# Kernel tuning notes

Hardware: AMD Instinct MI355X
Metric: run time of the kernel (lower is better)

The kernel has to match this reference:

```python
import jax, jax.numpy as jnp
import numpy as np

H, W = 16, 16  # input_resolution
NUM_HEADS = 16
DIM = 512


def build_relative_position_index(h, w):
    coords = np.stack(np.meshgrid(np.arange(h), np.arange(w), indexing='ij'))  # [2,h,w]
    cf = coords.reshape(2, -1)
    rel = cf[:, :, None] - cf[:, None, :]            # [2,N,N]
    rel = rel.transpose(1, 2, 0).astype(np.int32)    # [N,N,2]
    rel[:, :, 0] += h - 1
    rel[:, :, 1] += w - 1
    rel[:, :, 0] *= 2 * w - 1
    return jnp.asarray(rel.sum(-1).reshape(-1), dtype=jnp.int32)  # [N*N]


def setup_inputs() -> dict:
    key = jax.random.key(0)
    ks = jax.random.split(key, 6)
    B, N, C = 128, H * W, DIM
    x = jax.random.normal(ks[0], (B, N, C), dtype=jnp.float32)
    qkv_w = jax.random.normal(ks[1], (3 * C, C), dtype=jnp.float32) * (C ** -0.5)
    qkv_b = jax.random.normal(ks[2], (3 * C,), dtype=jnp.float32) * 0.02
    proj_w = jax.random.normal(ks[3], (C, C), dtype=jnp.float32) * (C ** -0.5)
    proj_b = jax.random.normal(ks[4], (C,), dtype=jnp.float32) * 0.02
    bias_table = jax.random.normal(ks[5], ((2 * H - 1) * (2 * W - 1), NUM_HEADS), dtype=jnp.float32) * 0.02
    rel_index = build_relative_position_index(H, W)
    return {"x": x, "qkv_w": qkv_w, "qkv_b": qkv_b, "proj_w": proj_w,
            "proj_b": proj_b, "bias_table": bias_table, "rel_index": rel_index}


def reference(x, qkv_w, qkv_b, proj_w, proj_b, bias_table, rel_index):
    B, N, C = x.shape
    h = NUM_HEADS
    hd = C // h
    scale = hd ** -0.5
    # qkv projection: [B,N,3C] -> [3,B,h,N,hd]
    qkv = (jnp.einsum('bnc,oc->bno', x, qkv_w) + qkv_b)
    qkv = qkv.reshape(B, N, 3, h, hd).transpose(2, 0, 3, 1, 4)
    q, k, v = qkv[0], qkv[1], qkv[2]
    # relative position bias: gather [N*N,h] -> [1,h,N,N]
    bias = bias_table[rel_index].reshape(N, N, h).transpose(2, 0, 1)[None]
    attn = jnp.einsum('bhnd,bhmd->bhnm', q * scale, k) + bias
    attn = jax.nn.softmax(attn, axis=-1)
    out = jnp.einsum('bhnm,bhmd->bhnd', attn, v)     # [B,h,N,hd]
    out = out.transpose(0, 2, 1, 3).reshape(B, N, C)
    return jnp.einsum('bnc,oc->bno', out, proj_w) + proj_b
```

## Files before the change

### kernel.cpp

```cpp
#include <hip/hip_runtime.h>

typedef __bf16 bf16_t;
typedef __bf16 bf16x4 __attribute__((ext_vector_type(4)));
typedef __bf16 bf16x8 __attribute__((ext_vector_type(8)));
typedef float f32x4 __attribute__((ext_vector_type(4)));

#define MFMA_16x16x32(a, b, c) __builtin_amdgcn_mfma_f32_16x16x32_bf16((a), (b), (c), 0, 0, 0)
#define LOG2E 1.4426950408889634f

__device__ inline bf16x8 cvt8(const float* __restrict__ p) {
  bf16x8 r;
#pragma unroll
  for (int j = 0; j < 8; j++) r[j] = (bf16_t)p[j];
  return r;
}

__device__ inline void load_lds16(const bf16_t* g, bf16_t* l) {
  __builtin_amdgcn_global_load_lds(
      (const __attribute__((address_space(1))) void*)g,
      (__attribute__((address_space(3))) void*)l, 16, 0, 0);
}

__global__ __launch_bounds__(256) void prep_k(
    const float* __restrict__ x, const float* __restrict__ qkv_w,
    const float* __restrict__ proj_w, const float* __restrict__ table,
    const int* __restrict__ rel,
    bf16_t* __restrict__ xbf, bf16_t* __restrict__ wqkvbf,
    bf16_t* __restrict__ wprojbf, float* __restrict__ biasws) {
  const int bid = blockIdx.x;
  if (bid < 8704) {
    size_t base = ((size_t)bid * 256 + threadIdx.x) * 8;
    if (base < 16777216) {
      *(bf16x8*)(xbf + base) = cvt8(x + base);
    } else if (base < 17563648) {
      size_t o = base - 16777216;
      *(bf16x8*)(wqkvbf + o) = cvt8(qkv_w + o);
    } else {
      size_t o = base - 17563648;
      *(bf16x8*)(wprojbf + o) = cvt8(proj_w + o);
    }
  } else {
    int idx = (bid - 8704) * 256 + threadIdx.x;
    int h = idx >> 16;
    int rem = idx & 65535;
    int rb = rem >> 12;
    int ct = (rem >> 8) & 15;
    int L = (rem >> 2) & 63;
    int r = idx & 3;
    int row = rb * 16 + (L >> 4) * 4 + r;
    int col = ct * 16 + (L & 15);
    biasws[idx] = table[rel[row * 256 + col] * 16 + h] * LOG2E;
  }
}

#define PH_OPEN() __builtin_amdgcn_s_setprio(1)

#define PH_CLOSE()                                        \
  do {                                                    \
    __builtin_amdgcn_s_setprio(0);                        \
    asm volatile("s_waitcnt lgkmcnt(0)" ::: "memory");    \
    __builtin_amdgcn_sched_barrier(0);                    \
    __builtin_amdgcn_s_barrier();                         \
    __builtin_amdgcn_sched_barrier(0);                    \
  } while (0)

#define GATE4()                                           \
  do {                                                    \
    __builtin_amdgcn_s_setprio(0);                        \
    asm volatile("s_waitcnt vmcnt(4)" ::: "memory");      \
    __builtin_amdgcn_s_barrier();                         \
    __builtin_amdgcn_sched_barrier(0);                    \
  } while (0)

#define GATE0()                                           \
  do {                                                    \
    __builtin_amdgcn_s_setprio(0);                        \
    asm volatile("s_waitcnt vmcnt(0)" ::: "memory");      \
    __builtin_amdgcn_s_barrier();                         \
    __builtin_amdgcn_sched_barrier(0);                    \
  } while (0)

#define STG2(src, dst, c)                                                        \
  do {                                                                           \
    load_lds16((src) + (c)*16384, (dst) + (c)*2048);                             \
    load_lds16((src) + ((c) + 1) * 16384, (dst) + ((c) + 1) * 2048);             \
  } while (0)

#define RDA2(dst, buf, ibase)                                                    \
  _Pragma("unroll") for (int i = 0; i < 2; ++i) {                                \
    dst[i][0] = *(const bf16x8*)&As[(buf)*8192 + a0 + ((ibase) + i) * 1024];     \
    dst[i][1] = *(const bf16x8*)&As[(buf)*8192 + a1 + ((ibase) + i) * 1024];     \
  }
#define RDB2(dst, buf, jbase)                                                    \
  _Pragma("unroll") for (int j = 0; j < 2; ++j) {                                \
    dst[j][0] = *(const bf16x8*)&Bs[(buf)*8192 + b0 + ((jbase) + j) * 1024];     \
    dst[j][1] = *(const bf16x8*)&Bs[(buf)*8192 + b1 + ((jbase) + j) * 1024];     \
  }

#define MFQ2(Af, Bf, I0, J0)                                                     \
  _Pragma("unroll") for (int i = 0; i < 2; ++i) _Pragma("unroll")                \
      for (int j = 0; j < 2; ++j) {                                              \
    acc[(I0) + i][(J0) + j] =                                                    \
        MFMA_16x16x32(Af[i][0], Bf[j][0], acc[(I0) + i][(J0) + j]);              \
    acc[(I0) + i][(J0) + j] =                                                    \
        MFMA_16x16x32(Af[i][1], Bf[j][1], acc[(I0) + i][(J0) + j]);              \
  }

#define GEMM_SETUP(Ap, Wp)                                                       \
  __shared__ bf16_t As[2 * 8192];                                                \
  __shared__ bf16_t Bs[2 * 8192];                                                \
  const int t = threadIdx.x;                                                     \
  const int w = t >> 6, L = t & 63;                                              \
  const int wm = w >> 1, wn = w & 1;                                             \
  const int lrow = L & 15, lq = L >> 4;                                          \
  const int srow = t >> 3;                                                       \
  const int sslot = (t & 7) ^ (srow & 7);                                        \
  const bf16_t* ga = (Ap) + (size_t)(m0 + srow) * 512 + sslot * 8;               \
  const bf16_t* gb = (Wp) + (size_t)(n0 + srow) * 512 + sslot * 8;               \
  bf16_t* la = As + t * 8;                                                       \
  bf16_t* lb = Bs + t * 8;                                                       \
  const int m8 = (lrow & 7) * 8;                                                 \
  const int a0 = (wm * 64 + lrow) * 64 + ((lq * 8) ^ m8);                        \
  const int a1 = (wm * 64 + lrow) * 64 + ((32 + lq * 8) ^ m8);                   \
  const int b0 = (wn * 64 + lrow) * 64 + ((lq * 8) ^ m8);                        \
  const int b1 = (wn * 64 + lrow) * 64 + ((32 + lq * 8) ^ m8);

#define PROLOGUE()                                                               \
  STG2(ga, la, 0); STG2(ga, la, 2);                                              \
  STG2(gb, lb, 0); STG2(gb, lb, 2);                                              \
  STG2(ga + 64, la + 8192, 0); STG2(ga + 64, la + 8192, 2);                      \
  asm volatile("s_waitcnt vmcnt(4)" ::: "memory");                               \
  __builtin_amdgcn_s_barrier();                                                  \
  __builtin_amdgcn_sched_barrier(0);

#define HALF_STEADY(CUR, LBDST, LADST, GBP, GAP)                                 \
  {                                                                              \
    bf16x8 fal[2][2], fbl[2][2], fah[2][2], fbh[2][2];                           \
    RDA2(fal, CUR, 0); RDB2(fbl, CUR, 0); RDB2(fbh, CUR, 2);                     \
    STG2(GBP, LBDST, 0);                                                         \
    PH_OPEN(); MFQ2(fal, fbl, 0, 0); PH_CLOSE();                                 \
    RDA2(fah, CUR, 2);                                                           \
    STG2(GBP, LBDST, 2);                                                         \
    PH_OPEN(); MFQ2(fal, fbh, 0, 2); PH_CLOSE();                                 \
    STG2(GAP, LADST, 0);                                                         \
    PH_OPEN(); MFQ2(fah, fbh, 2, 2); PH_CLOSE();                                 \
    STG2(GAP, LADST, 2);                                                         \
    PH_OPEN(); MFQ2(fah, fbl, 2, 0); GATE4();                                    \
  }

#define GEMM_LOOP()                                                              \
  {                                                                              \
    const bf16_t* gA = ga + 128;                                       \
    const bf16_t* gB = gb + 64;                                        \
    _Pragma("unroll 1") for (int G = 0; G < 3; ++G) {                            \
      HALF_STEADY(0, lb + 8192, la, gB, gA)                                      \
      HALF_STEADY(1, lb, la + 8192, gB + 64, gA + 64)                            \
      gA += 128; gB += 128;                                                      \
    }                                                                            \
    {            \
      bf16x8 fal[2][2], fbl[2][2], fah[2][2], fbh[2][2];                         \
      RDA2(fal, 0, 0); RDB2(fbl, 0, 0); RDB2(fbh, 0, 2);                         \
      STG2(gB, lb + 8192, 0);                                                    \
      PH_OPEN(); MFQ2(fal, fbl, 0, 0); PH_CLOSE();                               \
      RDA2(fah, 0, 2);                                                           \
      STG2(gB, lb + 8192, 2);                                                    \
      PH_OPEN(); MFQ2(fal, fbh, 0, 2); PH_CLOSE();                               \
      PH_OPEN(); MFQ2(fah, fbh, 2, 2); PH_CLOSE();                               \
      PH_OPEN(); MFQ2(fah, fbl, 2, 0); GATE0();                                  \
    }                                                                            \
    {                               \
      bf16x8 fal[2][2], fbl[2][2], fah[2][2], fbh[2][2];                         \
      RDA2(fal, 1, 0); RDB2(fbl, 1, 0); RDB2(fbh, 1, 2);                         \
      PH_OPEN(); MFQ2(fal, fbl, 0, 0); PH_CLOSE();                               \
      RDA2(fah, 1, 2);                                                           \
      PH_OPEN(); MFQ2(fal, fbh, 0, 2); PH_CLOSE();                               \
      PH_OPEN(); MFQ2(fah, fbh, 2, 2); PH_CLOSE();                               \
      PH_OPEN(); MFQ2(fah, fbl, 2, 0);                                           \
      __builtin_amdgcn_s_setprio(0);                                             \
      __builtin_amdgcn_sched_barrier(0);                                         \
    }                                                                            \
  }

__global__ __launch_bounds__(256, 2) void qkv_gemm128_k(
    const bf16_t* __restrict__ A, const bf16_t* __restrict__ W,
    const float* __restrict__ Bvec,
    bf16_t* __restrict__ qws, bf16_t* __restrict__ kws, bf16_t* __restrict__ vws) {
  const int id = blockIdx.x;
  const int wg = (id & 7) * 384 + (id >> 3);
  const int mt = wg / 12, nt = wg % 12;
  const int m0 = mt * 128, n0 = nt * 128;

  GEMM_SETUP(A, W);

  f32x4 acc[4][4];
#pragma unroll
  for (int jj = 0; jj < 4; ++jj) {
    float bv = Bvec[n0 + wn * 64 + jj * 16 + lrow];
#pragma unroll
    for (int i = 0; i < 4; ++i) acc[i][jj] = (f32x4){bv, bv, bv, bv};
  }

  PROLOGUE();
  GEMM_LOOP();

  const int col0 = n0 + wn * 64;
  const int s = col0 >> 9;
  bf16_t* dst = (s == 0) ? qws : (s == 1) ? kws : vws;
  const float mul = (s == 0) ? 0.17677669529663687f * LOG2E : 1.0f;
#pragma unroll
  for (int jj = 0; jj < 4; ++jj) {
    int o = col0 + jj * 16 + lrow;
    int rem = o & 511;
    int hh = rem >> 5, d = rem & 31;
#pragma unroll
    for (int i = 0; i < 4; ++i) {
#pragma unroll
      for (int r = 0; r < 4; ++r) {
        int m = m0 + wm * 64 + i * 16 + lq * 4 + r;
        int b = m >> 8, n = m & 255;
        dst[(size_t)(((b * 16 + hh) * 256 + n) << 5) + d] =
            (bf16_t)(acc[i][jj][r] * mul);
      }
    }
  }
}

__global__ __launch_bounds__(256, 2) void proj_gemm128_k(
    const bf16_t* __restrict__ A, const bf16_t* __restrict__ W,
    const float* __restrict__ Bvec, float* __restrict__ out) {
  const int id = blockIdx.x;
  const int wg = (id & 7) * 128 + (id >> 3);
  const int mt = wg >> 2, nt = wg & 3;
  const int m0 = mt * 128, n0 = nt * 128;

  GEMM_SETUP(A, W);

  f32x4 acc[4][4];
#pragma unroll
  for (int jj = 0; jj < 4; ++jj) {
    float bv = Bvec[n0 + wn * 64 + jj * 16 + lrow];
#pragma unroll
    for (int i = 0; i < 4; ++i) acc[i][jj] = (f32x4){bv, bv, bv, bv};
  }

  PROLOGUE();
  GEMM_LOOP();

#pragma unroll
  for (int jj = 0; jj < 4; ++jj) {
    int o = n0 + wn * 64 + jj * 16 + lrow;
#pragma unroll
    for (int i = 0; i < 4; ++i) {
#pragma unroll
      for (int r = 0; r < 4; ++r) {
        int m = m0 + wm * 64 + i * 16 + lq * 4 + r;
        out[(size_t)m * 512 + o] = acc[i][jj][r];
      }
    }
  }
}

__global__ __launch_bounds__(256) void attn_k(
    const bf16_t* __restrict__ qws, const bf16_t* __restrict__ kws,
    const bf16_t* __restrict__ vws, const float* __restrict__ biasws,
    bf16_t* __restrict__ aows) {
  __shared__ __align__(16) char smem[33792 + 16896];
  bf16_t* Ps = (bf16_t*)smem;
  bf16_t* Vs = (bf16_t*)(smem + 33792);

  const int id = blockIdx.x;
  const int xcd = id & 7;
  const int jj = id >> 3;
  const int bh = (jj >> 2) * 8 + xcd;
  const int strip = jj & 3;
  const int h = bh & 15, b = bh >> 4;

  const int t = threadIdx.x;
  const int w = t >> 6, L = t & 63;
  const int lrow = L & 15, lq = L >> 4;

  const bf16_t* kbase = kws + (size_t)bh * 8192;
  const bf16_t* vbase = vws + (size_t)bh * 8192;
#pragma unroll
  for (int c = 0; c < 4; c++) {
    bf16x8 vv = *(const bf16x8*)(vbase + t * 32 + c * 8);
#pragma unroll
    for (int j = 0; j < 8; j++) Vs[(c * 8 + j) * 264 + t] = vv[j];
  }

  const bf16_t* qbase = qws + (size_t)bh * 8192 + (strip * 64 + w * 16) * 32;
  bf16x8 qf = *(const bf16x8*)(qbase + lrow * 32 + lq * 8);
  bf16x8 kf[16];
#pragma unroll
  for (int ct = 0; ct < 16; ct++)
    kf[ct] = *(const bf16x8*)(kbase + (ct * 16 + lrow) * 32 + lq * 8);

  const float* bb = biasws + h * 65536 + (strip * 4 + w) * 4096;
  f32x4 S[16];
  __builtin_amdgcn_s_setprio(1);
#pragma unroll
  for (int ct = 0; ct < 16; ct++) {
    f32x4 bi = *(const f32x4*)(bb + ct * 256 + L * 4);
    S[ct] = MFMA_16x16x32(qf, kf[ct], bi);
  }
  __builtin_amdgcn_s_setprio(0);

  float sm[4] = {0.f, 0.f, 0.f, 0.f};
#pragma unroll
  for (int ct = 0; ct < 16; ct++)
#pragma unroll
    for (int r = 0; r < 4; r++) {
      float e;
      asm("v_exp_f32 %0, %1" : "=v"(e) : "v"(S[ct][r]));
      S[ct][r] = e;
      sm[r] += e;
    }
#pragma unroll
  for (int r = 0; r < 4; r++)
#pragma unroll
    for (int msk = 1; msk < 16; msk <<= 1)
      sm[r] += __shfl_xor(sm[r], msk, 64);

  const int srcb = ((lrow >> 2) * 16) * 4;
  float d0 = __int_as_float(__builtin_amdgcn_ds_bpermute(srcb, __float_as_int(sm[0])));
  float d1 = __int_as_float(__builtin_amdgcn_ds_bpermute(srcb, __float_as_int(sm[1])));
  float d2 = __int_as_float(__builtin_amdgcn_ds_bpermute(srcb, __float_as_int(sm[2])));
  float d3 = __int_as_float(__builtin_amdgcn_ds_bpermute(srcb, __float_as_int(sm[3])));
  const int rsel = lrow & 3;
  float den = (rsel == 0) ? d0 : (rsel == 1) ? d1 : (rsel == 2) ? d2 : d3;
  const float invq = 1.0f / den;

  bf16_t* Pw = Ps + w * 4224;
#pragma unroll
  for (int ct = 0; ct < 16; ct++)
#pragma unroll
    for (int r = 0; r < 4; r++)
      Pw[(lq * 4 + r) * 264 + ct * 16 + lrow] = (bf16_t)S[ct][r];

  __syncthreads();

  f32x4 O0 = {}, O1 = {};
  __builtin_amdgcn_s_setprio(1);
#pragma unroll
  for (int c = 0; c < 8; c++) {
    bf16x8 pf = *(const bf16x8*)&Pw[lrow * 264 + c * 32 + lq * 8];
    bf16x8 v0 = *(const bf16x8*)&Vs[lrow * 264 + c * 32 + lq * 8];
    bf16x8 v1 = *(const bf16x8*)&Vs[(16 + lrow) * 264 + c * 32 + lq * 8];
    O0 = MFMA_16x16x32(v0, pf, O0);
    O1 = MFMA_16x16x32(v1, pf, O1);
  }
  __builtin_amdgcn_s_setprio(0);

  bf16_t* orow = aows + (size_t)(b * 256 + strip * 64 + w * 16 + lrow) * 512 + h * 32;
  bf16x4 s0, s1;
#pragma unroll
  for (int r = 0; r < 4; r++) {
    s0[r] = (bf16_t)(O0[r] * invq);
    s1[r] = (bf16_t)(O1[r] * invq);
  }
  *(bf16x4*)(orow + lq * 4) = s0;
  *(bf16x4*)(orow + 16 + lq * 4) = s1;
}

extern "C" void kernel_launch(void* const* d_in, const int* in_sizes, int n_in,
                              void* d_out, int out_size, void* d_ws, size_t ws_size,
                              hipStream_t stream) {
  (void)in_sizes; (void)n_in; (void)out_size; (void)ws_size;
  const float* x      = (const float*)d_in[0];
  const float* qkv_w  = (const float*)d_in[1];
  const float* qkv_b  = (const float*)d_in[2];
  const float* proj_w = (const float*)d_in[3];
  const float* proj_b = (const float*)d_in[4];
  const float* table  = (const float*)d_in[5];
  const int*   rel    = (const int*)d_in[6];

  const size_t QKV_ELEMS = 16777216;
  bf16_t* qws     = (bf16_t*)d_ws;
  bf16_t* kws     = qws + QKV_ELEMS;
  bf16_t* vws     = kws + QKV_ELEMS;
  float*  biasws  = (float*)(vws + QKV_ELEMS);
  bf16_t* wqkvbf  = (bf16_t*)(biasws + 1048576);
  bf16_t* wprojbf = wqkvbf + 786432;
  bf16_t* xbf     = wprojbf + 262144;
  bf16_t* aows    = xbf;
  float*  out     = (float*)d_out;

  prep_k<<<12800, 256, 0, stream>>>(x, qkv_w, proj_w, table, rel,
                                    xbf, wqkvbf, wprojbf, biasws);
  qkv_gemm128_k<<<3072, 256, 0, stream>>>(xbf, wqkvbf, qkv_b, qws, kws, vws);
  attn_k<<<8192, 256, 0, stream>>>(qws, kws, vws, biasws, aows);
  proj_gemm128_k<<<1024, 256, 0, stream>>>(aows, wprojbf, proj_b, out);
}
```

Baseline: 280.1 us.

## Store V pre-transposed and swizzled, load to LDS directly, halve P buffer

The QKV GEMM epilogue now writes V in a transposed [d][n] layout with an XOR swizzle on 8-element groups. That lets the attention kernel copy V into LDS with direct global-to-LDS loads instead of a register transpose. The P staging buffer is also halved by processing the 256 keys in two halves, which cuts LDS use per block and may allow more blocks to be resident. In exchange, the V epilogue stores become more scattered, and an extra write/read round trip to LDS per half is added.

Measured after the change: 289.2 us. 3.3% more time.

```diff
diff --git a/kernel.cpp b/kernel.cpp
--- a/kernel.cpp
+++ b/kernel.cpp
@@ -205,21 +205,42 @@
 
   const int col0 = n0 + wn * 64;
   const int s = col0 >> 9;
-  bf16_t* dst = (s == 0) ? qws : (s == 1) ? kws : vws;
-  const float mul = (s == 0) ? 0.17677669529663687f * LOG2E : 1.0f;
-#pragma unroll
-  for (int jj = 0; jj < 4; ++jj) {
-    int o = col0 + jj * 16 + lrow;
-    int rem = o & 511;
-    int hh = rem >> 5, d = rem & 31;
-#pragma unroll
-    for (int i = 0; i < 4; ++i) {
-#pragma unroll
-      for (int r = 0; r < 4; ++r) {
-        int m = m0 + wm * 64 + i * 16 + lq * 4 + r;
-        int b = m >> 8, n = m & 255;
-        dst[(size_t)(((b * 16 + hh) * 256 + n) << 5) + d] =
-            (bf16_t)(acc[i][jj][r] * mul);
+  if (s == 2) {
+#pragma unroll
+    for (int jj = 0; jj < 4; ++jj) {
+      int o = col0 + jj * 16 + lrow;
+      int rem = o & 511;
+      int hh = rem >> 5, d = rem & 31;
+      int dx = d & 7;
+#pragma unroll
+      for (int i = 0; i < 4; ++i) {
+#pragma unroll
+        for (int r = 0; r < 4; ++r) {
+          int m = m0 + wm * 64 + i * 16 + lq * 4 + r;
+          int b = m >> 8, n = m & 255;
+          int p = (n >> 3) ^ dx;
+          vws[(size_t)(b * 16 + hh) * 8192 + d * 256 + p * 8 + (n & 7)] =
+              (bf16_t)acc[i][jj][r];
+        }
+      }
+    }
+  } else {
+    bf16_t* dst = (s == 0) ? qws : kws;
+    const float mul = (s == 0) ? 0.17677669529663687f * LOG2E : 1.0f;
+#pragma unroll
+    for (int jj = 0; jj < 4; ++jj) {
+      int o = col0 + jj * 16 + lrow;
+      int rem = o & 511;
+      int hh = rem >> 5, d = rem & 31;
+#pragma unroll
+      for (int i = 0; i < 4; ++i) {
+#pragma unroll
+        for (int r = 0; r < 4; ++r) {
+          int m = m0 + wm * 64 + i * 16 + lq * 4 + r;
+          int b = m >> 8, n = m & 255;
+          dst[(size_t)(((b * 16 + hh) * 256 + n) << 5) + d] =
+              (bf16_t)(acc[i][jj][r] * mul);
+        }
       }
     }
   }
@@ -264,9 +285,9 @@
     const bf16_t* __restrict__ qws, const bf16_t* __restrict__ kws,
     const bf16_t* __restrict__ vws, const float* __restrict__ biasws,
     bf16_t* __restrict__ aows) {
-  __shared__ __align__(16) char smem[33792 + 16896];
+  __shared__ __align__(16) char smem[17408 + 16384];
   bf16_t* Ps = (bf16_t*)smem;
-  bf16_t* Vs = (bf16_t*)(smem + 33792);
+  bf16_t* VsL = (bf16_t*)(smem + 17408);
 
   const int id = blockIdx.x;
   const int xcd = id & 7;
@@ -279,15 +300,13 @@
   const int w = t >> 6, L = t & 63;
   const int lrow = L & 15, lq = L >> 4;
 
+  const bf16_t* vtb = vws + (size_t)bh * 8192;
+  load_lds16(vtb + t * 8, VsL + t * 8);
+  load_lds16(vtb + 2048 + t * 8, VsL + 2048 + t * 8);
+  load_lds16(vtb + 4096 + t * 8, VsL + 4096 + t * 8);
+  load_lds16(vtb + 6144 + t * 8, VsL + 6144 + t * 8);
+
   const bf16_t* kbase = kws + (size_t)bh * 8192;
-  const bf16_t* vbase = vws + (size_t)bh * 8192;
-#pragma unroll
-  for (int c = 0; c < 4; c++) {
-    bf16x8 vv = *(const bf16x8*)(vbase + t * 32 + c * 8);
-#pragma unroll
-    for (int j = 0; j < 8; j++) Vs[(c * 8 + j) * 264 + t] = vv[j];
-  }
-
   const bf16_t* qbase = qws + (size_t)bh * 8192 + (strip * 64 + w * 16) * 32;
   bf16x8 qf = *(const bf16x8*)(qbase + lrow * 32 + lq * 8);
   bf16x8 kf[16];
@@ -330,26 +349,33 @@
   float den = (rsel == 0) ? d0 : (rsel == 1) ? d1 : (rsel == 2) ? d2 : d3;
   const float invq = 1.0f / den;
 
-  bf16_t* Pw = Ps + w * 4224;
-#pragma unroll
-  for (int ct = 0; ct < 16; ct++)
-#pragma unroll
-    for (int r = 0; r < 4; r++)
-      Pw[(lq * 4 + r) * 264 + ct * 16 + lrow] = (bf16_t)S[ct][r];
-
+  asm volatile("s_waitcnt vmcnt(0)" ::: "memory");
   __syncthreads();
 
   f32x4 O0 = {}, O1 = {};
-  __builtin_amdgcn_s_setprio(1);
-#pragma unroll
-  for (int c = 0; c < 8; c++) {
-    bf16x8 pf = *(const bf16x8*)&Pw[lrow * 264 + c * 32 + lq * 8];
-    bf16x8 v0 = *(const bf16x8*)&Vs[lrow * 264 + c * 32 + lq * 8];
-    bf16x8 v1 = *(const bf16x8*)&Vs[(16 + lrow) * 264 + c * 32 + lq * 8];
-    O0 = MFMA_16x16x32(v0, pf, O0);
-    O1 = MFMA_16x16x32(v1, pf, O1);
-  }
-  __builtin_amdgcn_s_setprio(0);
+  bf16_t* Pw = Ps + w * 2176;
+  const int xr = lrow & 7;
+#pragma unroll
+  for (int hf = 0; hf < 2; ++hf) {
+#pragma unroll
+    for (int cti = 0; cti < 8; ++cti) {
+      int ct = hf * 8 + cti;
+#pragma unroll
+      for (int r = 0; r < 4; ++r)
+        Pw[(lq * 4 + r) * 136 + cti * 16 + lrow] = (bf16_t)S[ct][r];
+    }
+    __builtin_amdgcn_s_setprio(1);
+#pragma unroll
+    for (int c = 0; c < 4; ++c) {
+      int sl = (((hf * 4 + c) * 4 + lq) ^ xr) * 8;
+      bf16x8 pf = *(const bf16x8*)&Pw[lrow * 136 + c * 32 + lq * 8];
+      bf16x8 v0 = *(const bf16x8*)&VsL[lrow * 256 + sl];
+      bf16x8 v1 = *(const bf16x8*)&VsL[(16 + lrow) * 256 + sl];
+      O0 = MFMA_16x16x32(v0, pf, O0);
+      O1 = MFMA_16x16x32(v1, pf, O1);
+    }
+    __builtin_amdgcn_s_setprio(0);
+  }
 
   bf16_t* orow = aows + (size_t)(b * 256 + strip * 64 + w * 16 + lrow) * 512 + h * 32;
   bf16x4 s0, s1;
```
